# Kernel optimization log

Hardware: AMD Instinct MI355X
Metric: run time of the kernel (lower is better)

## Reference

```python
import jax, jax.numpy as jnp
import numpy as np

B, N, C = 2, 2048, 768
H = 12
HD = C // H
SCALE = HD ** -0.5


def setup_inputs() -> dict:
    key = jax.random.key(0)
    ks = jax.random.split(key, 5)
    s = 1.0 / np.sqrt(C)
    return {
        "x": jax.random.normal(ks[0], (B, N, C), dtype=jnp.float32),
        "Wq": jax.random.normal(ks[1], (C, C), dtype=jnp.float32) * s,
        "Wk": jax.random.normal(ks[2], (C, C), dtype=jnp.float32) * s,
        "Wv": jax.random.normal(ks[3], (C, C), dtype=jnp.float32) * s,
        "Wo": jax.random.normal(ks[4], (C, C), dtype=jnp.float32) * s,
        "bo": jnp.zeros((C,), dtype=jnp.float32),
    }


def reference(x, Wq, Wk, Wv, Wo, bo):
    b, n, c = x.shape
    # projections (equinox Linear: y = W @ x, i.e. x @ W.T); split heads -> [b, h, n, hd]
    q = (x @ Wq.T).reshape(b, n, H, HD).transpose(0, 2, 1, 3)
    k = (x @ Wk.T).reshape(b, n, H, HD).transpose(0, 2, 1, 3)
    v = (x @ Wv.T).reshape(b, n, H, HD).transpose(0, 2, 1, 3)
    # full O(N^2) score matrix, scaled dot-product
    scores = jnp.einsum("bhqd,bhkd->bhqk", q, k) * SCALE  # [b, h, n, n]
    probs = jax.nn.softmax(scores, axis=-1)
    # attn_drop = 0.0 -> identity
    out = jnp.einsum("bhqk,bhkd->bhqd", probs, v)  # [b, h, n, hd]
    out = out.transpose(0, 2, 1, 3).reshape(b, n, c)
    # output projection (proj_drop = 0.0 -> identity)
    return out @ Wo.T + bo
```

## Files before the change

### kernel.cpp

```cpp
#include <hip/hip_runtime.h>
#include <hip/hip_bf16.h>
#include <cstdint>

typedef __bf16 bf16;
typedef bf16 bf16x8 __attribute__((ext_vector_type(8)));
typedef float f32x4 __attribute__((ext_vector_type(4)));
typedef uint32_t u32;

#define MFMA16(a, b, c) __builtin_amdgcn_mfma_f32_16x16x32_bf16(a, b, c, 0, 0, 0)

static constexpr int Bb = 2, Hh = 12, Nn = 2048, Cc = 768, HD = 64;
static constexpr float SCALE_L2E = 0.125f * 1.4426950408889634f;

__device__ inline u32 pkbf(float a, float b) {
    union { struct { uint16_t lo, hi; } s; u32 w; } u;
    u.s.lo = __builtin_bit_cast(uint16_t, (bf16)a);
    u.s.hi = __builtin_bit_cast(uint16_t, (bf16)b);
    return u.w;
}

__device__ __forceinline__ size_t fidx(int bh, int n, int hd) {
    return ((size_t)(bh * 128 + (n >> 4)) * 2 + (hd >> 5)) * 512 +
           (size_t)(((hd >> 3) & 3) * 128 + (n & 15) * 8 + (hd & 7));
}
__device__ __forceinline__ size_t vidx(int bh, int n, int hd) {
    return (((size_t)(bh * 32 + (n >> 6)) * 4 + (hd >> 4)) * 2 + ((n >> 5) & 1)) * 512 +
           (size_t)(((n >> 3) & 3) * 128 + (hd & 15) * 8 + (n & 7));
}

__device__ __forceinline__ void stage16(const bf16* g, bf16* l) {
    __builtin_amdgcn_global_load_lds(
        (const __attribute__((address_space(1))) void*)g,
        (__attribute__((address_space(3))) void*)l, 16, 0, 0);
}

__device__ __forceinline__ void gload(bf16x8& d, const bf16* p) {
    asm volatile("global_load_dwordx4 %0, %1, off" : "=v"(d) : "v"(p));
}

#define VMWAIT(N) do { asm volatile("s_waitcnt vmcnt(" #N ")" ::); \
                       __builtin_amdgcn_sched_barrier(0); } while (0)

__global__ __launch_bounds__(256) void cvt_all(const float* __restrict__ x,
                                               const float* __restrict__ wq,
                                               const float* __restrict__ wk,
                                               const float* __restrict__ wv,
                                               const float* __restrict__ wo,
                                               bf16* __restrict__ xb,
                                               bf16* __restrict__ wqkv,
                                               bf16* __restrict__ wob) {
    const int b = blockIdx.x;
    const float* src;
    bf16* dst;
    int i;
    if (b < 1536) {
        src = x; dst = xb; i = b * 256 + threadIdx.x;
    } else {
        const int wbid  = b - 1536;
        const int which = wbid / 288;
        src = which == 0 ? wq : which == 1 ? wk : which == 2 ? wv : wo;
        dst = which == 3 ? wob : wqkv + (size_t)which * 589824;
        i = (wbid % 288) * 256 + threadIdx.x;
    }
    const float4* p = reinterpret_cast<const float4*>(src) + (size_t)i * 2;
    float4 v0 = p[0], v1 = p[1];
    bf16x8 o;
    o[0] = (bf16)v0.x; o[1] = (bf16)v0.y; o[2] = (bf16)v0.z; o[3] = (bf16)v0.w;
    o[4] = (bf16)v1.x; o[5] = (bf16)v1.y; o[6] = (bf16)v1.z; o[7] = (bf16)v1.w;
    reinterpret_cast<bf16x8*>(dst)[i] = o;
}

__global__ __launch_bounds__(256, 3) void gemm_qkv(const bf16* __restrict__ X,
                                                   const bf16* __restrict__ W,
                                                   bf16* __restrict__ QF,
                                                   bf16* __restrict__ KF,
                                                   bf16* __restrict__ VF) {
    const int m0      = blockIdx.x * 128;
    const int j00     = blockIdx.y * 128;
    const int grp     = blockIdx.y / 6;
    const int colbase = (blockIdx.y % 6) * 128;
    const int w   = threadIdx.x >> 6;
    const int wr  = w >> 1;
    const int wc  = w & 1;
    const int l   = threadIdx.x & 63;
    const int lr  = l & 15;
    const int lg  = l >> 4;

    __shared__ bf16 lsA[2][128 * 32];
    __shared__ bf16 lsB[2][128 * 32];

    const int lrow = l >> 2;
    const int lcol = (l & 3) * 8;

    auto STAGE = [&](int buf, int kk) {
#pragma unroll
        for (int i = 0; i < 2; i++) {
            const int s = w * 2 + i;
            stage16(X + (size_t)(m0 + s * 16 + lrow) * Cc + kk + lcol, &lsA[buf][s * 512]);
            stage16(W + (size_t)(j00 + s * 16 + lrow) * Cc + kk + lcol, &lsB[buf][s * 512]);
        }
    };

    f32x4 acc[4][4] = {};

    STAGE(0, 0);
    __syncthreads();
    int cur = 0;
#pragma unroll 1
    for (int it = 0; it < 24; ++it) {
        if (it < 23) STAGE(cur ^ 1, (it + 1) * 32);
        bf16x8 a[4], b[4];
#pragma unroll
        for (int r = 0; r < 4; r++)
            a[r] = *reinterpret_cast<const bf16x8*>(&lsA[cur][(wr * 64 + r * 16 + lr) * 32 + lg * 8]);
#pragma unroll
        for (int c = 0; c < 4; c++)
            b[c] = *reinterpret_cast<const bf16x8*>(&lsB[cur][(wc * 64 + c * 16 + lr) * 32 + lg * 8]);
        __builtin_amdgcn_s_setprio(1);
#pragma unroll
        for (int r = 0; r < 4; r++)
#pragma unroll
            for (int c = 0; c < 4; c++)
                acc[r][c] = MFMA16(a[r], b[c], acc[r][c]);
        __builtin_amdgcn_s_setprio(0);
        __syncthreads();
        cur ^= 1;
    }

#pragma unroll
    for (int r = 0; r < 4; r++)
#pragma unroll
        for (int c = 0; c < 4; c++)
#pragma unroll
            for (int j = 0; j < 4; j++) {
                const int m   = m0 + wr * 64 + r * 16 + lg * 4 + j;
                const int col = colbase + wc * 64 + c * 16 + lr;
                const int bb = m >> 11, n = m & 2047;
                const int h = col >> 6, hd = col & 63;
                const int bh = bb * Hh + h;
                const float v = acc[r][c][j];
                if (grp == 0) {
                    QF[fidx(bh, n, hd)] = (bf16)(v * SCALE_L2E);
                } else if (grp == 1) {
                    KF[fidx(bh, n, hd)] = (bf16)v;
                } else {
                    VF[vidx(bh, n, hd)] = (bf16)v;
                }
            }
}

__global__ __launch_bounds__(256) void gemm_proj(const bf16* __restrict__ X,
                                                 const bf16* __restrict__ W,
                                                 const float* __restrict__ bias,
                                                 float* __restrict__ Y) {
    const int m0 = blockIdx.x * 64;
    const int j0 = blockIdx.y * 64;
    const int w  = threadIdx.x >> 6;
    const int l  = threadIdx.x & 63;
    const int lr = l & 15;
    const int lg = l >> 4;

    __shared__ bf16 lsA[2][64 * 32];
    __shared__ bf16 lsB[2][64 * 32];

    const int lrow = l >> 2;
    const int lcol = (l & 3) * 8;

    auto STAGE = [&](int buf, int kk) {
        stage16(X + (size_t)(m0 + w * 16 + lrow) * Cc + kk + lcol, &lsA[buf][w * 512]);
        stage16(W + (size_t)(j0 + w * 16 + lrow) * Cc + kk + lcol, &lsB[buf][w * 512]);
    };

    f32x4 acc[4] = {};

    STAGE(0, 0);
    __syncthreads();
    int cur = 0;
#pragma unroll 1
    for (int it = 0; it < 24; ++it) {
        if (it < 23) STAGE(cur ^ 1, (it + 1) * 32);
        bf16x8 a = *reinterpret_cast<const bf16x8*>(&lsA[cur][(w * 16 + lr) * 32 + lg * 8]);
        bf16x8 b[4];
#pragma unroll
        for (int c = 0; c < 4; c++)
            b[c] = *reinterpret_cast<const bf16x8*>(&lsB[cur][(c * 16 + lr) * 32 + lg * 8]);
        __builtin_amdgcn_s_setprio(1);
#pragma unroll
        for (int c = 0; c < 4; c++)
            acc[c] = MFMA16(a, b[c], acc[c]);
        __builtin_amdgcn_s_setprio(0);
        __syncthreads();
        cur ^= 1;
    }

    const int mw = m0 + w * 16;
#pragma unroll
    for (int c = 0; c < 4; c++)
#pragma unroll
        for (int j = 0; j < 4; j++) {
            const int m   = mw + lg * 4 + j;
            const int col = j0 + c * 16 + lr;
            Y[(size_t)m * Cc + col] = acc[c][j] + bias[col];
        }
}

__global__ __launch_bounds__(512, 4) void attn_kernel(const bf16* __restrict__ QF,
                                                      const bf16* __restrict__ KF,
                                                      const bf16* __restrict__ VF,
                                                      bf16* __restrict__ AO) {
    const int bid  = (blockIdx.x & 7) * 96 + (blockIdx.x >> 3);
    const int qb   = bid & 31;
    const int bh   = bid >> 5;
    const int tid  = threadIdx.x;
    const int wid  = tid >> 6;
    const int team = wid >> 2;
    const int wt   = wid & 3;
    const int l    = tid & 63;
    const int lr   = l & 15;
    const int lg   = l >> 4;

    __shared__ bf16 vbuf[2][2][4096];
    __shared__ u32  p_lds[8][576];

    f32x4 acc[4] = {};
    f32x4 accs = {0.f, 0.f, 0.f, 0.f};

    const bf16* Qp = QF + ((size_t)(bh * 128 + qb * 4 + wt) * 2) * 512 + l * 8;
    const bf16x8 qf0 = *reinterpret_cast<const bf16x8*>(Qp);
    const bf16x8 qf1 = *reinterpret_cast<const bf16x8*>(Qp + 512);

    bf16x8 ONES;
#pragma unroll
    for (int i = 0; i < 8; i++) ONES[i] = (bf16)1.0f;

    bf16x8 ka[8];

    const int tbase = team * 16;

    auto loadK = [&](int t) {
        const bf16* p = KF + ((size_t)bh * 256 + (tbase + t) * 8) * 512 + l * 8;
#pragma unroll
        for (int s = 0; s < 8; s++)
            gload(ka[s], p + (size_t)s * 512);
    };
    auto stageV = [&](int slot, int t) {
        const size_t tb = ((size_t)bh * 256 + (tbase + t) * 8) * 512;
#pragma unroll
        for (int i = 0; i < 2; i++) {
            const int s = wt * 2 + i;
            stage16(VF + tb + (size_t)s * 512 + l * 8, &vbuf[team][slot][s * 512]);
        }
    };

    const f32x4 fz = {0.f, 0.f, 0.f, 0.f};

    stageV(0, 0);
    loadK(0);

#pragma unroll 1
    for (int t = 0; t < 16; ++t) {
        VMWAIT(0);
        __builtin_amdgcn_s_barrier();

        f32x4 s[4];
        __builtin_amdgcn_s_setprio(1);
#pragma unroll
        for (int st = 0; st < 4; st++) {
            s[st] = MFMA16(ka[st * 2], qf0, fz);
            s[st] = MFMA16(ka[st * 2 + 1], qf1, s[st]);
        }
        __builtin_amdgcn_s_setprio(0);
        if (t < 15) {
            loadK(t + 1);
            stageV((t + 1) & 1, t + 1);
        }

#pragma unroll
        for (int st = 0; st < 4; st++) {
            float p0 = exp2f(s[st][0]);
            float p1 = exp2f(s[st][1]);
            float p2 = exp2f(s[st][2]);
            float p3 = exp2f(s[st][3]);
            *reinterpret_cast<uint2*>(&p_lds[wid][lr * 36 + st * 8 + lg * 2]) =
                make_uint2(pkbf(p0, p1), pkbf(p2, p3));
        }
        asm volatile("s_waitcnt lgkmcnt(0)" ::: "memory");
        __builtin_amdgcn_sched_barrier(0);
        const bf16x8 pa0 = *reinterpret_cast<const bf16x8*>(&p_lds[wid][lr * 36 + lg * 4]);
        const bf16x8 pa1 = *reinterpret_cast<const bf16x8*>(&p_lds[wid][lr * 36 + 16 + lg * 4]);

        const bf16* vb = &vbuf[team][t & 1][l * 8];
        __builtin_amdgcn_s_setprio(1);
#pragma unroll
        for (int c = 0; c < 4; c++) {
            bf16x8 v0 = *reinterpret_cast<const bf16x8*>(vb + (c * 2) * 512);
            bf16x8 v1 = *reinterpret_cast<const bf16x8*>(vb + (c * 2 + 1) * 512);
            acc[c] = MFMA16(v0, pa0, acc[c]);
            acc[c] = MFMA16(v1, pa1, acc[c]);
        }
        accs = MFMA16(ONES, pa0, accs);
        accs = MFMA16(ONES, pa1, accs);
        __builtin_amdgcn_s_setprio(0);
    }

    __syncthreads();
    float* mrg = reinterpret_cast<float*>(&p_lds[0][0]);
    if (team == 1) {
        float* slot = mrg + wt * 1088 + l * 17;
#pragma unroll
        for (int c = 0; c < 4; c++)
#pragma unroll
            for (int j = 0; j < 4; j++) slot[c * 4 + j] = acc[c][j];
        slot[16] = accs[0];
    }
    __syncthreads();
    if (team == 1) return;

    const float* slot = mrg + wt * 1088 + l * 17;
#pragma unroll
    for (int c = 0; c < 4; c++)
#pragma unroll
        for (int j = 0; j < 4; j++) acc[c][j] += slot[c * 4 + j];
    const float rtot = accs[0] + slot[16];

    float* o_lds = reinterpret_cast<float*>(&vbuf[0][0][0]) + wt * 1088;
    const float rinv = 1.0f / rtot;
#pragma unroll
    for (int c = 0; c < 4; c++)
#pragma unroll
        for (int j = 0; j < 4; j++)
            o_lds[(c * 16 + lg * 4 + j) * 17 + lr] = acc[c][j] * rinv;
    asm volatile("s_waitcnt lgkmcnt(0)" ::: "memory");
    __builtin_amdgcn_sched_barrier(0);

    const int bb = bh / Hh, h = bh % Hh;
    const int q0 = qb * 64 + wt * 16;
    const int qq = l >> 2, dc = (l & 3) * 16;
    bf16x8 o0, o1;
#pragma unroll
    for (int dd = 0; dd < 8; dd++) o0[dd] = (bf16)o_lds[(dc + dd) * 17 + qq];
#pragma unroll
    for (int dd = 0; dd < 8; dd++) o1[dd] = (bf16)o_lds[(dc + 8 + dd) * 17 + qq];
    bf16* dst = AO + ((size_t)(bb * Nn) + q0 + qq) * Cc + h * 64 + dc;
    *reinterpret_cast<bf16x8*>(dst) = o0;
    *reinterpret_cast<bf16x8*>(dst + 8) = o1;
}

extern "C" void kernel_launch(void* const* d_in, const int* in_sizes, int n_in,
                              void* d_out, int out_size, void* d_ws, size_t ws_size,
                              hipStream_t stream) {
    const float* x  = (const float*)d_in[0];
    const float* Wq = (const float*)d_in[1];
    const float* Wk = (const float*)d_in[2];
    const float* Wv = (const float*)d_in[3];
    const float* Wo = (const float*)d_in[4];
    const float* bo = (const float*)d_in[5];

    const size_t XB    = 0;
    const size_t WQKVB = XB + 6291456;
    const size_t WOB   = WQKVB + 3538944;
    const size_t QB    = WOB + 1179648;
    const size_t KB    = QB + 6291456;
    const size_t VTB   = KB + 6291456;
    const size_t AOB   = VTB + 6291456;
    const size_t NEED  = AOB + 6291456;
    if (ws_size < NEED) return;

    char* ws = (char*)d_ws;
    bf16* xb   = (bf16*)(ws + XB);
    bf16* wqkv = (bf16*)(ws + WQKVB);
    bf16* wob  = (bf16*)(ws + WOB);
    bf16* QF   = (bf16*)(ws + QB);
    bf16* KF   = (bf16*)(ws + KB);
    bf16* VF   = (bf16*)(ws + VTB);
    bf16* AOb  = (bf16*)(ws + AOB);

    cvt_all<<<2688, 256, 0, stream>>>(x, Wq, Wk, Wv, Wo, xb, wqkv, wob);

    gemm_qkv<<<dim3(32, 18), 256, 0, stream>>>(xb, wqkv, QF, KF, VF);

    attn_kernel<<<768, 512, 0, stream>>>(QF, KF, VF, AOb);

    gemm_proj<<<dim3(64, 12), 256, 0, stream>>>(AOb, wob, bo, (float*)d_out);
}
```

Measured before the change: 101.8 us.

## Process two query fragments per wave in attention to reuse K/V loads

```diff
diff --git a/kernel.cpp b/kernel.cpp
--- a/kernel.cpp
+++ b/kernel.cpp
@@ -204,7 +204,7 @@
         }
 }
 
-__global__ __launch_bounds__(512, 4) void attn_kernel(const bf16* __restrict__ QF,
+__global__ __launch_bounds__(256, 3) void attn_kernel(const bf16* __restrict__ QF,
                                                       const bf16* __restrict__ KF,
                                                       const bf16* __restrict__ VF,
                                                       bf16* __restrict__ AO) {
@@ -213,28 +213,29 @@
     const int bh   = bid >> 5;
     const int tid  = threadIdx.x;
     const int wid  = tid >> 6;
-    const int team = wid >> 2;
-    const int wt   = wid & 3;
+    const int team = wid >> 1;
+    const int wt   = wid & 1;
     const int l    = tid & 63;
     const int lr   = l & 15;
     const int lg   = l >> 4;
 
     __shared__ bf16 vbuf[2][2][4096];
-    __shared__ u32  p_lds[8][576];
-
-    f32x4 acc[4] = {};
-    f32x4 accs = {0.f, 0.f, 0.f, 0.f};
-
-    const bf16* Qp = QF + ((size_t)(bh * 128 + qb * 4 + wt) * 2) * 512 + l * 8;
-    const bf16x8 qf0 = *reinterpret_cast<const bf16x8*>(Qp);
-    const bf16x8 qf1 = *reinterpret_cast<const bf16x8*>(Qp + 512);
+    __shared__ u32  p_lds[4][2][576];
+
+    f32x4 acc[2][4] = {};
+    f32x4 accs[2] = {};
+
+    const bf16* Qbase = QF + ((size_t)(bh * 128 + qb * 4 + wt * 2) * 2) * 512 + l * 8;
+    const bf16x8 qa0 = *reinterpret_cast<const bf16x8*>(Qbase);
+    const bf16x8 qb0 = *reinterpret_cast<const bf16x8*>(Qbase + 512);
+    const bf16x8 qa1 = *reinterpret_cast<const bf16x8*>(Qbase + 1024);
+    const bf16x8 qb1 = *reinterpret_cast<const bf16x8*>(Qbase + 1536);
 
     bf16x8 ONES;
 #pragma unroll
     for (int i = 0; i < 8; i++) ONES[i] = (bf16)1.0f;
 
     bf16x8 ka[8];
-
     const int tbase = team * 16;
 
     auto loadK = [&](int t) {
@@ -246,48 +247,62 @@
     auto stageV = [&](int slot, int t) {
         const size_t tb = ((size_t)bh * 256 + (tbase + t) * 8) * 512;
 #pragma unroll
-        for (int i = 0; i < 2; i++) {
-            const int s = wt * 2 + i;
+        for (int i = 0; i < 4; i++) {
+            const int s = wt * 4 + i;
             stage16(VF + tb + (size_t)s * 512 + l * 8, &vbuf[team][slot][s * 512]);
         }
     };
 
     const f32x4 fz = {0.f, 0.f, 0.f, 0.f};
 
-    stageV(0, 0);
-    loadK(0);
-
-#pragma unroll 1
-    for (int t = 0; t < 16; ++t) {
-        VMWAIT(0);
-        __builtin_amdgcn_s_barrier();
-
-        f32x4 s[4];
-        __builtin_amdgcn_s_setprio(1);
-#pragma unroll
-        for (int st = 0; st < 4; st++) {
-            s[st] = MFMA16(ka[st * 2], qf0, fz);
-            s[st] = MFMA16(ka[st * 2 + 1], qf1, s[st]);
-        }
-        __builtin_amdgcn_s_setprio(0);
-        if (t < 15) {
-            loadK(t + 1);
-            stageV((t + 1) & 1, t + 1);
-        }
-
+    auto EXPPACK = [&](int f, const f32x4* s) {
 #pragma unroll
         for (int st = 0; st < 4; st++) {
             float p0 = exp2f(s[st][0]);
             float p1 = exp2f(s[st][1]);
             float p2 = exp2f(s[st][2]);
             float p3 = exp2f(s[st][3]);
-            *reinterpret_cast<uint2*>(&p_lds[wid][lr * 36 + st * 8 + lg * 2]) =
+            *reinterpret_cast<uint2*>(&p_lds[wid][f][lr * 36 + st * 8 + lg * 2]) =
                 make_uint2(pkbf(p0, p1), pkbf(p2, p3));
         }
+    };
+
+    stageV(0, 0);
+    loadK(0);
+
+#pragma unroll 1
+    for (int t = 0; t < 16; ++t) {
+        VMWAIT(0);
+        __builtin_amdgcn_s_barrier();
+
+        f32x4 s[4];
+        __builtin_amdgcn_s_setprio(1);
+#pragma unroll
+        for (int st = 0; st < 4; st++) {
+            s[st] = MFMA16(ka[st * 2], qa0, fz);
+            s[st] = MFMA16(ka[st * 2 + 1], qb0, s[st]);
+        }
+        __builtin_amdgcn_s_setprio(0);
+        EXPPACK(0, s);
+        __builtin_amdgcn_s_setprio(1);
+#pragma unroll
+        for (int st = 0; st < 4; st++) {
+            s[st] = MFMA16(ka[st * 2], qa1, fz);
+            s[st] = MFMA16(ka[st * 2 + 1], qb1, s[st]);
+        }
+        __builtin_amdgcn_s_setprio(0);
+        if (t < 15) {
+            loadK(t + 1);
+            stageV((t + 1) & 1, t + 1);
+        }
+        EXPPACK(1, s);
+
         asm volatile("s_waitcnt lgkmcnt(0)" ::: "memory");
         __builtin_amdgcn_sched_barrier(0);
-        const bf16x8 pa0 = *reinterpret_cast<const bf16x8*>(&p_lds[wid][lr * 36 + lg * 4]);
-        const bf16x8 pa1 = *reinterpret_cast<const bf16x8*>(&p_lds[wid][lr * 36 + 16 + lg * 4]);
+        const bf16x8 pa00 = *reinterpret_cast<const bf16x8*>(&p_lds[wid][0][lr * 36 + lg * 4]);
+        const bf16x8 pa01 = *reinterpret_cast<const bf16x8*>(&p_lds[wid][0][lr * 36 + 16 + lg * 4]);
+        const bf16x8 pa10 = *reinterpret_cast<const bf16x8*>(&p_lds[wid][1][lr * 36 + lg * 4]);
+        const bf16x8 pa11 = *reinterpret_cast<const bf16x8*>(&p_lds[wid][1][lr * 36 + 16 + lg * 4]);
 
         const bf16* vb = &vbuf[team][t & 1][l * 8];
         __builtin_amdgcn_s_setprio(1);
@@ -295,55 +310,65 @@
         for (int c = 0; c < 4; c++) {
             bf16x8 v0 = *reinterpret_cast<const bf16x8*>(vb + (c * 2) * 512);
             bf16x8 v1 = *reinterpret_cast<const bf16x8*>(vb + (c * 2 + 1) * 512);
-            acc[c] = MFMA16(v0, pa0, acc[c]);
-            acc[c] = MFMA16(v1, pa1, acc[c]);
-        }
-        accs = MFMA16(ONES, pa0, accs);
-        accs = MFMA16(ONES, pa1, accs);
+            acc[0][c] = MFMA16(v0, pa00, acc[0][c]);
+            acc[0][c] = MFMA16(v1, pa01, acc[0][c]);
+            acc[1][c] = MFMA16(v0, pa10, acc[1][c]);
+            acc[1][c] = MFMA16(v1, pa11, acc[1][c]);
+        }
+        accs[0] = MFMA16(ONES, pa00, accs[0]);
+        accs[0] = MFMA16(ONES, pa01, accs[0]);
+        accs[1] = MFMA16(ONES, pa10, accs[1]);
+        accs[1] = MFMA16(ONES, pa11, accs[1]);
         __builtin_amdgcn_s_setprio(0);
     }
 
     __syncthreads();
-    float* mrg = reinterpret_cast<float*>(&p_lds[0][0]);
+    float* mrg = reinterpret_cast<float*>(&p_lds[0][0][0]);
     if (team == 1) {
-        float* slot = mrg + wt * 1088 + l * 17;
-#pragma unroll
-        for (int c = 0; c < 4; c++)
-#pragma unroll
-            for (int j = 0; j < 4; j++) slot[c * 4 + j] = acc[c][j];
-        slot[16] = accs[0];
+#pragma unroll
+        for (int f = 0; f < 2; f++) {
+            float* slot = mrg + (wt * 2 + f) * 1088 + l * 17;
+#pragma unroll
+            for (int c = 0; c < 4; c++)
+#pragma unroll
+                for (int j = 0; j < 4; j++) slot[c * 4 + j] = acc[f][c][j];
+            slot[16] = accs[f][0];
+        }
     }
     __syncthreads();
     if (team == 1) return;
 
-    const float* slot = mrg + wt * 1088 + l * 17;
-#pragma unroll
-    for (int c = 0; c < 4; c++)
-#pragma unroll
-        for (int j = 0; j < 4; j++) acc[c][j] += slot[c * 4 + j];
-    const float rtot = accs[0] + slot[16];
-
-    float* o_lds = reinterpret_cast<float*>(&vbuf[0][0][0]) + wt * 1088;
-    const float rinv = 1.0f / rtot;
-#pragma unroll
-    for (int c = 0; c < 4; c++)
-#pragma unroll
-        for (int j = 0; j < 4; j++)
-            o_lds[(c * 16 + lg * 4 + j) * 17 + lr] = acc[c][j] * rinv;
-    asm volatile("s_waitcnt lgkmcnt(0)" ::: "memory");
-    __builtin_amdgcn_sched_barrier(0);
-
     const int bb = bh / Hh, h = bh % Hh;
-    const int q0 = qb * 64 + wt * 16;
-    const int qq = l >> 2, dc = (l & 3) * 16;
-    bf16x8 o0, o1;
-#pragma unroll
-    for (int dd = 0; dd < 8; dd++) o0[dd] = (bf16)o_lds[(dc + dd) * 17 + qq];
-#pragma unroll
-    for (int dd = 0; dd < 8; dd++) o1[dd] = (bf16)o_lds[(dc + 8 + dd) * 17 + qq];
-    bf16* dst = AO + ((size_t)(bb * Nn) + q0 + qq) * Cc + h * 64 + dc;
-    *reinterpret_cast<bf16x8*>(dst) = o0;
-    *reinterpret_cast<bf16x8*>(dst + 8) = o1;
+#pragma unroll
+    for (int f = 0; f < 2; f++) {
+        const float* slot = mrg + (wt * 2 + f) * 1088 + l * 17;
+#pragma unroll
+        for (int c = 0; c < 4; c++)
+#pragma unroll
+            for (int j = 0; j < 4; j++) acc[f][c][j] += slot[c * 4 + j];
+        const float rtot = accs[f][0] + slot[16];
+        const float rinv = 1.0f / rtot;
+
+        float* o_lds = reinterpret_cast<float*>(&vbuf[0][0][0]) + (wt * 2 + f) * 1088;
+#pragma unroll
+        for (int c = 0; c < 4; c++)
+#pragma unroll
+            for (int j = 0; j < 4; j++)
+                o_lds[(c * 16 + lg * 4 + j) * 17 + lr] = acc[f][c][j] * rinv;
+        asm volatile("s_waitcnt lgkmcnt(0)" ::: "memory");
+        __builtin_amdgcn_sched_barrier(0);
+
+        const int q0 = qb * 64 + (wt * 2 + f) * 16;
+        const int qq = l >> 2, dc = (l & 3) * 16;
+        bf16x8 o0, o1;
+#pragma unroll
+        for (int dd = 0; dd < 8; dd++) o0[dd] = (bf16)o_lds[(dc + dd) * 17 + qq];
+#pragma unroll
+        for (int dd = 0; dd < 8; dd++) o1[dd] = (bf16)o_lds[(dc + 8 + dd) * 17 + qq];
+        bf16* dst = AO + ((size_t)(bb * Nn) + q0 + qq) * Cc + h * 64 + dc;
+        *reinterpret_cast<bf16x8*>(dst) = o0;
+        *reinterpret_cast<bf16x8*>(dst + 8) = o1;
+    }
 }
 
 extern "C" void kernel_launch(void* const* d_in, const int* in_sizes, int n_in,
@@ -379,7 +404,7 @@
 
     gemm_qkv<<<dim3(32, 18), 256, 0, stream>>>(xb, wqkv, QF, KF, VF);
 
-    attn_kernel<<<768, 512, 0, stream>>>(QF, KF, VF, AOb);
+    attn_kernel<<<768, 256, 0, stream>>>(QF, KF, VF, AOb);
 
     gemm_proj<<<dim3(64, 12), 256, 0, stream>>>(AOb, wob, bo, (float*)d_out);
 }
```

New measurement: 97.02 us. 4.7% less time.
